# Kernel tuning notes

Hardware: AMD Instinct MI355X
Metric: run time of the kernel (lower is better)

## Reference

```python
import jax, jax.numpy as jnp
import numpy as np

B, IN_CH, D, H, W = 2, 4, 8, 224, 224
DS = 4
DIM, HEADS, HEAD_DIM, LAYERS = 256, 8, 32, 4
INNER = HEADS * HEAD_DIM
MLP = 4 * DIM
WS = (4, 8, 8)
SHIFT = (2, 4, 4)
WVOL = WS[0] * WS[1] * WS[2]
Hp, Wp = H // DS, W // DS
NW = (D // WS[0]) * (Hp // WS[1]) * (Wp // WS[2])
NBIAS = (2 * WS[0] - 1) * (2 * WS[1] - 1) * (2 * WS[2] - 1)


def _rel_index():
    c = np.stack(np.meshgrid(np.arange(WS[0]), np.arange(WS[1]), np.arange(WS[2]), indexing='ij')).reshape(3, -1)
    r = (c[:, :, None] - c[:, None, :]).transpose(1, 2, 0)
    r[..., 0] += WS[0] - 1
    r[..., 1] += WS[1] - 1
    r[..., 2] += WS[2] - 1
    return r[..., 0] * (2 * WS[1] - 1) * (2 * WS[2] - 1) + r[..., 1] * (2 * WS[2] - 1) + r[..., 2]

REL_IDX = jnp.asarray(_rel_index())  # (WVOL, WVOL)


def _shift_mask():
    # standard Swin shifted-window attention mask on the post-merge grid
    img = np.zeros((D, Hp, Wp), np.int32)
    cnt = 0
    sl = lambda w, s: (slice(0, -w), slice(-w, -s), slice(-s, None))
    for sd in sl(WS[0], SHIFT[0]):
        for sh in sl(WS[1], SHIFT[1]):
            for sw in sl(WS[2], SHIFT[2]):
                img[sd, sh, sw] = cnt
                cnt += 1
    m = img.reshape(D // WS[0], WS[0], Hp // WS[1], WS[1], Wp // WS[2], WS[2])
    m = m.transpose(0, 2, 4, 1, 3, 5).reshape(NW, WVOL)
    return jnp.asarray(np.where(m[:, None, :] != m[:, :, None], -1e9, 0.0).astype(np.float32))

ATTN_MASK = _shift_mask()  # (NW, WVOL, WVOL)


def layer_norm(x, s, b):
    mu = x.mean(-1, keepdims=True)
    var = x.var(-1, keepdims=True)
    return (x - mu) / jnp.sqrt(var + 1e-5) * s + b


def window_attention(x, qkv_w, out_w, out_b, bias_tab, shifted):
    # x: (B, D, Hp, Wp, C) channel-last
    if shifted:
        x = jnp.roll(x, (-SHIFT[0], -SHIFT[1], -SHIFT[2]), axis=(1, 2, 3))
    xw = x.reshape(B, D // WS[0], WS[0], Hp // WS[1], WS[1], Wp // WS[2], WS[2], DIM)
    xw = xw.transpose(0, 1, 3, 5, 2, 4, 6, 7).reshape(B, NW, WVOL, DIM)
    qkv = xw @ qkv_w  # (B, NW, WVOL, 3*INNER)
    q, k, v = jnp.split(qkv, 3, axis=-1)
    split = lambda t: t.reshape(B, NW, WVOL, HEADS, HEAD_DIM).transpose(0, 1, 3, 2, 4)
    q = split(q) * (HEAD_DIM ** -0.5)
    k, v = split(k), split(v)
    attn = jnp.einsum('bwhid,bwhjd->bwhij', q, k)  # (B, NW, H, WVOL, WVOL)
    bias = bias_tab[REL_IDX].transpose(2, 0, 1)  # (H, WVOL, WVOL)
    attn = attn + bias
    if shifted:
        attn = attn + ATTN_MASK[None, :, None]
    attn = jax.nn.softmax(attn, axis=-1)
    o = jnp.einsum('bwhij,bwhjd->bwhid', attn, v)
    o = o.transpose(0, 1, 3, 2, 4).reshape(B, NW, WVOL, INNER)
    o = o @ out_w + out_b
    o = o.reshape(B, D // WS[0], Hp // WS[1], Wp // WS[2], WS[0], WS[1], WS[2], DIM)
    o = o.transpose(0, 1, 4, 2, 5, 3, 6, 7).reshape(B, D, Hp, Wp, DIM)
    if shifted:
        o = jnp.roll(o, SHIFT, axis=(1, 2, 3))
    return o


def setup_inputs() -> dict:
    key = jax.random.key(0)
    ks = jax.random.split(key, 12)
    s = 0.02
    return {
        'x': jax.random.normal(ks[0], (B, IN_CH, D, H, W), jnp.float32),
        'conv_w': jax.random.normal(ks[1], (DIM, IN_CH, 1, DS, DS), jnp.float32) * s,
        'conv_b': jnp.zeros((DIM,), jnp.float32),
        'ln1_s': jnp.ones((LAYERS, DIM), jnp.float32),
        'ln1_b': jnp.zeros((LAYERS, DIM), jnp.float32),
        'qkv_w': jax.random.normal(ks[2], (LAYERS, DIM, 3 * INNER), jnp.float32) * s,
        'out_w': jax.random.normal(ks[3], (LAYERS, INNER, DIM), jnp.float32) * s,
        'out_b': jnp.zeros((LAYERS, DIM), jnp.float32),
        'bias_tab': jax.random.normal(ks[4], (LAYERS, NBIAS, HEADS), jnp.float32) * s,
        'ln2_s': jnp.ones((LAYERS, DIM), jnp.float32),
        'ln2_b': jnp.zeros((LAYERS, DIM), jnp.float32),
        'fc1_w': jax.random.normal(ks[5], (LAYERS, DIM, MLP), jnp.float32) * s,
        'fc1_b': jnp.zeros((LAYERS, MLP), jnp.float32),
        'fc2_w': jax.random.normal(ks[6], (LAYERS, MLP, DIM), jnp.float32) * s,
        'fc2_b': jnp.zeros((LAYERS, DIM), jnp.float32),
    }


def reference(x, conv_w, conv_b, ln1_s, ln1_b, qkv_w, out_w, out_b, bias_tab, ln2_s, ln2_b, fc1_w, fc1_b, fc2_w, fc2_b):
    # patch merge: Conv3d kernel (1, DS, DS) stride (1, DS, DS)
    y = jax.lax.conv_general_dilated(
        x, conv_w, window_strides=(1, DS, DS), padding='VALID',
        dimension_numbers=('NCDHW', 'OIDHW', 'NCDHW'))
    y = y + conv_b[None, :, None, None, None]
    y = y.transpose(0, 2, 3, 4, 1)  # (B, D, Hp, Wp, DIM) channel-last
    for i in range(LAYERS):
        shifted = (i % 2 == 1)
        y = y + window_attention(layer_norm(y, ln1_s[i], ln1_b[i]),
                                 qkv_w[i], out_w[i], out_b[i], bias_tab[i], shifted)
        h = layer_norm(y, ln2_s[i], ln2_b[i])
        h = jax.nn.gelu(h @ fc1_w[i] + fc1_b[i]) @ fc2_w[i] + fc2_b[i]
        y = y + h
    return y.transpose(0, 4, 1, 2, 3)  # (B, DIM, D, Hp, Wp)
```

## Files before the change

### kernel.cpp

```cpp
#include <hip/hip_runtime.h>

typedef unsigned short ushort_t;
typedef unsigned int   uint_t;

#define NTOK 50176
#define NWIN 98
#define NBIAS 1575

typedef __attribute__((ext_vector_type(8))) short bf16x8;
typedef __attribute__((ext_vector_type(4))) float floatx4;

static __device__ __forceinline__ float lo2f(uint_t u) { return __uint_as_float(u << 16); }
static __device__ __forceinline__ float hi2f(uint_t u) { return __uint_as_float(u & 0xffff0000u); }
static __device__ __forceinline__ ushort_t f2b(float f) {
    union { float f; uint_t u; } v; v.f = f;
    uint_t u = v.u + 0x7fffu + ((v.u >> 16) & 1u);
    return (ushort_t)(u >> 16);
}

__global__ void transpose_w(const float* __restrict__ src, ushort_t* __restrict__ dst,
                            int K, int N) {
    long base = (long)blockIdx.y * K * N;
    int idx = blockIdx.x * 256 + threadIdx.x;
    if (idx < K * N) {
        int k = idx / N, n = idx - k * N;
        dst[base + (long)n * K + k] = f2b(src[base + idx]);
    }
}

__global__ void cast_bf16(const float* __restrict__ src, ushort_t* __restrict__ dst, int n) {
    int i = blockIdx.x * 256 + threadIdx.x;
    if (i < n) dst[i] = f2b(src[i]);
}

__global__ void gen_btab(const float* __restrict__ bias_tab, float* __restrict__ Btab) {
    int slot = blockIdx.y;
    int layer, cls;
    if (slot == 0)      { layer = 0; cls = 0; }
    else if (slot < 9)  { layer = 1; cls = slot - 1; }
    else if (slot == 9) { layer = 2; cls = 0; }
    else                { layer = 3; cls = slot - 10; }
    int idx = blockIdx.x * 256 + threadIdx.x;
    int hd = idx >> 16;
    int ij = idx & 65535;
    int i = ij >> 8, j = ij & 255;
    int di = i >> 6, hi = (i >> 3) & 7, wi = i & 7;
    int dj = j >> 6, hj = (j >> 3) & 7, wj = j & 7;
    int rel = (di - dj + 3) * 225 + (hi - hj + 7) * 15 + (wi - wj + 7);
    float v = bias_tab[((long)layer * NBIAS + rel) * 8 + hd];
    int cd = cls >> 2, ch = (cls >> 1) & 1, cw = cls & 1;
    int ri = (cd ? (di < 2 ? 1 : 2) : 0) * 9 + (ch ? (hi < 4 ? 1 : 2) : 0) * 3 + (cw ? (wi < 4 ? 1 : 2) : 0);
    int rj = (cd ? (dj < 2 ? 1 : 2) : 0) * 9 + (ch ? (hj < 4 ? 1 : 2) : 0) * 3 + (cw ? (wj < 4 ? 1 : 2) : 0);
    if (ri != rj) v = -1e9f;
    Btab[(long)slot * 524288 + idx] = v * 1.4426950408889634f;
}

__global__ void im2row(const float* __restrict__ X, ushort_t* __restrict__ A) {
    int idx = blockIdx.x * 256 + threadIdx.x;
    int t = idx >> 4;
    int k = idx & 15;
    int ic = k >> 2, kh = k & 3;
    int w = t % 56, h = (t / 56) % 56, d = (t / 3136) % 8, b = t / 25088;
    long xi = (((long)(b * 4 + ic) * 8 + d) * 224 + (h * 4 + kh)) * 224 + w * 4;
    float4 u = *(const float4*)(X + xi);
    ushort_t* ap = A + (long)t * 64 + ic * 16 + kh * 4;
    ap[0] = f2b(u.x); ap[1] = f2b(u.y); ap[2] = f2b(u.z); ap[3] = f2b(u.w);
}

__global__ void ln_kernel(const float* __restrict__ Y, ushort_t* __restrict__ Xn,
                          const float* __restrict__ S, const float* __restrict__ Bb) {
    int wv = threadIdx.x >> 6, lane = threadIdx.x & 63;
    long t = (long)blockIdx.x * 4 + wv;
    const float* y = Y + t * 256;
    float v[4], s = 0.f, s2 = 0.f;
#pragma unroll
    for (int r = 0; r < 4; ++r) { v[r] = y[lane + 64 * r]; s += v[r]; s2 += v[r] * v[r]; }
#pragma unroll
    for (int off = 32; off; off >>= 1) { s += __shfl_xor(s, off, 64); s2 += __shfl_xor(s2, off, 64); }
    float mu = s * (1.f / 256.f);
    float var = s2 * (1.f / 256.f) - mu * mu;
    float rstd = rsqrtf(var + 1e-5f);
#pragma unroll
    for (int r = 0; r < 4; ++r) {
        int c = lane + 64 * r;
        Xn[t * 256 + c] = f2b((v[r] - mu) * rstd * S[c] + Bb[c]);
    }
}

__global__ __launch_bounds__(256, 2) void gemm_bt(
    const ushort_t* __restrict__ A, const ushort_t* __restrict__ BT,
    int M, int N, int K,
    const float* __restrict__ bias, int mode,
    ushort_t* __restrict__ C, float* __restrict__ Y) {
    __shared__ ushort_t As[128 * 32];
    __shared__ ushort_t Bs[128 * 32];
    const int tid = threadIdx.x;
    const int wv = tid >> 6;
    const int lane = tid & 63;
    const int quad = lane >> 4;
    const int l15 = lane & 15;
    const long m0 = (long)blockIdx.x * 128;
    const long n0 = (long)blockIdx.y * 128;
    const int wm = (wv & 1) * 64;
    const int wn = (wv >> 1) * 64;
    const int r_loc = lane >> 2;
    const int k_loc = (lane & 3) * 8;

    floatx4 acc[4][4] = {};

    const ushort_t* Ab = A + m0 * K;
    const ushort_t* Bb = BT + n0 * K;

    for (int kt = 0; kt < K; kt += 32) {
#pragma unroll
        for (int q = 0; q < 2; ++q) {
            int slot = wv * 2 + q;
            int row = slot * 16 + r_loc;
            __builtin_amdgcn_global_load_lds(
                (const __attribute__((address_space(1))) void*)(Ab + (long)row * K + kt + k_loc),
                (__attribute__((address_space(3))) void*)(As + slot * 512), 16, 0, 0);
            __builtin_amdgcn_global_load_lds(
                (const __attribute__((address_space(1))) void*)(Bb + (long)row * K + kt + k_loc),
                (__attribute__((address_space(3))) void*)(Bs + slot * 512), 16, 0, 0);
        }
        __syncthreads();
        bf16x8 af[4], bfr[4];
#pragma unroll
        for (int i = 0; i < 4; ++i) {
            af[i]  = *(const bf16x8*)(As + (wm + i * 16 + l15) * 32 + quad * 8);
            bfr[i] = *(const bf16x8*)(Bs + (wn + i * 16 + l15) * 32 + quad * 8);
        }
#pragma unroll
        for (int mi = 0; mi < 4; ++mi)
#pragma unroll
            for (int ni = 0; ni < 4; ++ni)
                acc[mi][ni] = __builtin_amdgcn_mfma_f32_16x16x32_bf16(af[mi], bfr[ni], acc[mi][ni], 0, 0, 0);
        __syncthreads();
    }

    if (mode == 2) {
#pragma unroll
        for (int mi = 0; mi < 4; ++mi)
#pragma unroll
            for (int ni = 0; ni < 4; ++ni) {
                long col = n0 + wn + ni * 16 + l15;
                float bv = bias[col];
#pragma unroll
                for (int r = 0; r < 4; ++r) {
                    long row = m0 + wm + mi * 16 + quad * 4 + r;
                    Y[row * N + col] += acc[mi][ni][r] + bv;
                }
            }
    } else if (mode == 3) {
#pragma unroll
        for (int mi = 0; mi < 4; ++mi)
#pragma unroll
            for (int ni = 0; ni < 4; ++ni) {
                long col = n0 + wn + ni * 16 + l15;
                float bv = bias[col];
#pragma unroll
                for (int r = 0; r < 4; ++r) {
                    long row = m0 + wm + mi * 16 + quad * 4 + r;
                    Y[row * N + col] = acc[mi][ni][r] + bv;
                }
            }
    } else {
#pragma unroll
        for (int mi = 0; mi < 4; ++mi)
#pragma unroll
            for (int ni = 0; ni < 4; ++ni) {
                long col = n0 + wn + ni * 16 + l15;
                float bv = bias ? bias[col] : 0.f;
#pragma unroll
                for (int r = 0; r < 4; ++r) {
                    long row = m0 + wm + mi * 16 + quad * 4 + r;
                    float v = acc[mi][ni][r] + bv;
                    if (mode == 1) {
                        float x3 = v * v * v;
                        v = 0.5f * v * (1.f + tanhf(0.7978845608028654f * (v + 0.044715f * x3)));
                    }
                    C[row * N + col] = f2b(v);
                }
            }
    }
}

#define PSTR 134
#define VTSTR 266
__global__ __launch_bounds__(256, 3) void attn_mfma(
    const ushort_t* __restrict__ QKV, ushort_t* __restrict__ O,
    const float* __restrict__ Btab, int shifted) {
    __shared__ ushort_t Ks[256 * 32];
    __shared__ ushort_t Vt[32 * VTSTR];
    __shared__ ushort_t Pl[4 * 16 * PSTR];
    __shared__ int tok_s[256];

    const int tid = threadIdx.x;
    const int wv = tid >> 6;
    const int lane = tid & 63;
    const int quad = lane >> 4;
    const int l15 = lane & 15;
    const int wdx = blockIdx.x, hd = blockIdx.y, b = blockIdx.z;
    const int wd = wdx / 49;
    const int wh = (wdx / 7) % 7;
    const int ww = wdx % 7;

    const int cls = shifted ? ((wd << 2) | ((wh == 6) << 1) | (ww == 6)) : 0;
    const float* bt = Btab + ((long)(cls * 8 + hd)) * 65536;

    {
        const int t = tid;
        const int di = t >> 6, hi = (t >> 3) & 7, wi = t & 7;
        const int d = wd * 4 + di, h = wh * 8 + hi, w = ww * 8 + wi;
        int d0 = d, h0 = h, w0 = w;
        if (shifted) { d0 = (d + 2) & 7; h0 = (h + 4) % 56; w0 = (w + 4) % 56; }
        const long tok = ((long)((b * 8 + d0) * 56 + h0)) * 56 + w0;
        tok_s[t] = (int)tok;
        const uint4* kp = (const uint4*)(QKV + tok * 768 + 256 + hd * 32);
        const uint4* vp = (const uint4*)(QKV + tok * 768 + 512 + hd * 32);
        uint4* kd = (uint4*)(Ks + t * 32);
#pragma unroll
        for (int p = 0; p < 4; ++p) kd[p] = kp[p];
#pragma unroll
        for (int p = 0; p < 4; ++p) {
            uint4 vvu = vp[p];
            uint_t uu[4] = {vvu.x, vvu.y, vvu.z, vvu.w};
#pragma unroll
            for (int e = 0; e < 4; ++e) {
                int dd = p * 8 + e * 2;
                Vt[dd * VTSTR + t]       = (ushort_t)(uu[e] & 0xffffu);
                Vt[(dd + 1) * VTSTR + t] = (ushort_t)(uu[e] >> 16);
            }
        }
    }
    __syncthreads();

    const float scale = 0.17677669529663687f * 1.4426950408889634f;
    ushort_t* Pw = Pl + wv * 16 * PSTR;

    for (int rg = 0; rg < 4; ++rg) {
        const int rti = wv * 4 + rg;
        bf16x8 aq;
        {
            int tq = tok_s[rti * 16 + l15];
            const uint4* qp = (const uint4*)(QKV + (long)tq * 768 + hd * 32 + quad * 8);
            union { uint4 u; bf16x8 v; } cv; cv.u = *qp; aq = cv.v;
        }
        const float* bp = bt + (long)(rti * 16 + quad * 4) * 256 + l15;
        floatx4 Sc[16];
        float m4[4] = {-3e38f, -3e38f, -3e38f, -3e38f};
#pragma unroll
        for (int hf = 0; hf < 2; ++hf) {
            float bb[8][4];
#pragma unroll
            for (int n8 = 0; n8 < 8; ++n8)
#pragma unroll
                for (int r = 0; r < 4; ++r)
                    bb[n8][r] = bp[r * 256 + (hf * 8 + n8) * 16];
#pragma unroll
            for (int n8 = 0; n8 < 8; ++n8) {
                const int nt = hf * 8 + n8;
                bf16x8 bk = *(const bf16x8*)(Ks + (nt * 16 + l15) * 32 + quad * 8);
                floatx4 z = {};
                Sc[nt] = __builtin_amdgcn_mfma_f32_16x16x32_bf16(aq, bk, z, 0, 0, 0);
            }
#pragma unroll
            for (int n8 = 0; n8 < 8; ++n8) {
                const int nt = hf * 8 + n8;
#pragma unroll
                for (int r = 0; r < 4; ++r) {
                    float s = fmaf(Sc[nt][r], scale, bb[n8][r]);
                    Sc[nt][r] = s;
                    m4[r] = fmaxf(m4[r], s);
                }
            }
        }
#pragma unroll
        for (int r = 0; r < 4; ++r) {
            m4[r] = fmaxf(m4[r], __shfl_xor(m4[r], 1));
            m4[r] = fmaxf(m4[r], __shfl_xor(m4[r], 2));
            m4[r] = fmaxf(m4[r], __shfl_xor(m4[r], 4));
            m4[r] = fmaxf(m4[r], __shfl_xor(m4[r], 8));
        }
        float l4[4] = {0.f, 0.f, 0.f, 0.f};
#pragma unroll
        for (int nt = 0; nt < 16; ++nt)
#pragma unroll
            for (int r = 0; r < 4; ++r) {
                float p = __builtin_amdgcn_exp2f(Sc[nt][r] - m4[r]);
                l4[r] += p;
                Sc[nt][r] = p;
            }
#pragma unroll
        for (int r = 0; r < 4; ++r) {
            l4[r] += __shfl_xor(l4[r], 1);
            l4[r] += __shfl_xor(l4[r], 2);
            l4[r] += __shfl_xor(l4[r], 4);
            l4[r] += __shfl_xor(l4[r], 8);
        }
        float inv4[4];
#pragma unroll
        for (int r = 0; r < 4; ++r) inv4[r] = 1.f / l4[r];

        floatx4 oa[2] = {};
#pragma unroll
        for (int hf = 0; hf < 2; ++hf) {
#pragma unroll
            for (int n8 = 0; n8 < 8; ++n8)
#pragma unroll
                for (int r = 0; r < 4; ++r)
                    Pw[(quad * 4 + r) * PSTR + n8 * 16 + l15] = f2b(Sc[hf * 8 + n8][r]);
            __builtin_amdgcn_s_waitcnt(0xC07F);
            __builtin_amdgcn_wave_barrier();
#pragma unroll
            for (int ct = 0; ct < 2; ++ct)
#pragma unroll
                for (int kt = 0; kt < 4; ++kt) {
                    bf16x8 ap = *(const bf16x8*)(Pw + l15 * PSTR + kt * 32 + quad * 8);
                    bf16x8 bv = *(const bf16x8*)(Vt + (ct * 16 + l15) * VTSTR + hf * 128 + kt * 32 + quad * 8);
                    oa[ct] = __builtin_amdgcn_mfma_f32_16x16x32_bf16(ap, bv, oa[ct], 0, 0, 0);
                }
            __builtin_amdgcn_s_waitcnt(0xC07F);
            __builtin_amdgcn_wave_barrier();
        }
#pragma unroll
        for (int ct = 0; ct < 2; ++ct)
#pragma unroll
            for (int r = 0; r < 4; ++r) {
                int i = rti * 16 + quad * 4 + r;
                long tq = tok_s[i];
                O[tq * 256 + hd * 32 + ct * 16 + l15] = f2b(oa[ct][r] * inv4[r]);
            }
    }
}

__global__ void out_permute(const float* __restrict__ Y, float* __restrict__ Out) {
    __shared__ float tile[64][65];
    const int t0 = blockIdx.x * 64;
    const int c0 = blockIdx.y * 64;
    const int tid = threadIdx.x;
    const int a = tid >> 6;
    const int bx = tid & 63;
#pragma unroll
    for (int s8 = 0; s8 < 16; ++s8) {
        int tt = a + s8 * 4;
        tile[tt][bx] = Y[(long)(t0 + tt) * 256 + c0 + bx];
    }
    __syncthreads();
#pragma unroll
    for (int s8 = 0; s8 < 16; ++s8) {
        int cc = a + s8 * 4;
        int tok = t0 + bx;
        int bb = tok / 25088;
        int rem = tok - bb * 25088;
        Out[((long)(bb * 256 + c0 + cc)) * 25088 + rem] = tile[bx][cc];
    }
}

extern "C" void kernel_launch(void* const* d_in, const int* in_sizes, int n_in,
                              void* d_out, int out_size, void* d_ws, size_t ws_size,
                              hipStream_t stream) {
    (void)in_sizes; (void)n_in; (void)out_size; (void)ws_size;
    const float* x        = (const float*)d_in[0];
    const float* conv_w   = (const float*)d_in[1];
    const float* conv_b   = (const float*)d_in[2];
    const float* ln1_s    = (const float*)d_in[3];
    const float* ln1_b    = (const float*)d_in[4];
    const float* qkv_w    = (const float*)d_in[5];
    const float* out_w    = (const float*)d_in[6];
    const float* out_b    = (const float*)d_in[7];
    const float* bias_tab = (const float*)d_in[8];
    const float* ln2_s    = (const float*)d_in[9];
    const float* ln2_b    = (const float*)d_in[10];
    const float* fc1_w    = (const float*)d_in[11];
    const float* fc1_b    = (const float*)d_in[12];
    const float* fc2_w    = (const float*)d_in[13];
    const float* fc2_b    = (const float*)d_in[14];
    float* out = (float*)d_out;

    char* ws = (char*)d_ws;
    float*    y    = (float*)ws;    ws += (size_t)NTOK * 256 * 4;
    ushort_t* big  = (ushort_t*)ws; ws += (size_t)NTOK * 1024 * 2;
    ushort_t* xob  = (ushort_t*)ws; ws += (size_t)NTOK * 256 * 2;
    ushort_t* bt_qkv = (ushort_t*)ws; ws += (size_t)4 * 768 * 256 * 2;
    ushort_t* bt_out = (ushort_t*)ws; ws += (size_t)4 * 256 * 256 * 2;
    ushort_t* bt_fc1 = (ushort_t*)ws; ws += (size_t)4 * 1024 * 256 * 2;
    ushort_t* bt_fc2 = (ushort_t*)ws; ws += (size_t)4 * 256 * 1024 * 2;
    ushort_t* cw_bf  = (ushort_t*)ws; ws += (size_t)256 * 64 * 2;
    float*    btab   = (float*)ws;  ws += (size_t)18 * 524288 * 4;

    transpose_w<<<dim3((256 * 768 + 255) / 256, 4), 256, 0, stream>>>(qkv_w, bt_qkv, 256, 768);
    transpose_w<<<dim3((256 * 256 + 255) / 256, 4), 256, 0, stream>>>(out_w, bt_out, 256, 256);
    transpose_w<<<dim3((256 * 1024 + 255) / 256, 4), 256, 0, stream>>>(fc1_w, bt_fc1, 256, 1024);
    transpose_w<<<dim3((1024 * 256 + 255) / 256, 4), 256, 0, stream>>>(fc2_w, bt_fc2, 1024, 256);
    gen_btab<<<dim3(2048, 18), 256, 0, stream>>>(bias_tab, btab);

    cast_bf16<<<(256 * 64 + 255) / 256, 256, 0, stream>>>(conv_w, cw_bf, 256 * 64);
    im2row<<<NTOK * 16 / 256, 256, 0, stream>>>(x, big);
    gemm_bt<<<dim3(NTOK / 128, 2), 256, 0, stream>>>(
        big, cw_bf, NTOK, 256, 64, conv_b, 3, nullptr, y);

    static const int base_slot[4] = {0, 1, 9, 10};
    for (int i = 0; i < 4; ++i) {
        int sh = i & 1;
        ln_kernel<<<NTOK / 4, 256, 0, stream>>>(y, xob, ln1_s + i * 256, ln1_b + i * 256);
        gemm_bt<<<dim3(NTOK / 128, 6), 256, 0, stream>>>(
            xob, bt_qkv + (size_t)i * 768 * 256, NTOK, 768, 256, nullptr, 0, big, nullptr);
        attn_mfma<<<dim3(NWIN, 8, 2), 256, 0, stream>>>(
            big, xob, btab + (size_t)base_slot[i] * 524288, sh);
        gemm_bt<<<dim3(NTOK / 128, 2), 256, 0, stream>>>(
            xob, bt_out + (size_t)i * 256 * 256, NTOK, 256, 256, out_b + i * 256, 2, nullptr, y);
        ln_kernel<<<NTOK / 4, 256, 0, stream>>>(y, xob, ln2_s + i * 256, ln2_b + i * 256);
        gemm_bt<<<dim3(NTOK / 128, 8), 256, 0, stream>>>(
            xob, bt_fc1 + (size_t)i * 1024 * 256, NTOK, 1024, 256, fc1_b + i * 1024, 1, big, nullptr);
        gemm_bt<<<dim3(NTOK / 128, 2), 256, 0, stream>>>(
            big, bt_fc2 + (size_t)i * 256 * 1024, NTOK, 256, 1024, fc2_b + i * 256, 2, nullptr, y);
    }

    out_permute<<<dim3(NTOK / 64, 4), 256, 0, stream>>>(y, out);
}
```

Baseline: 1.424 ms.

## Transpose QK^T MFMA so softmax rows live per lane with packed bf16 P stores

Swaps the MFMA operand order so each lane holds one query row's scores across its four accumulator elements. The row max and sum then need only two cross-lane shuffles instead of sixteen. Bias is loaded as float4 vectors, and P is written to LDS with packed v_cvt_pk_bf16_f32 as 64-bit stores using a tighter row stride. The normalisation factor is redistributed with extra shuffles, and the change to LDS padding may alter bank-conflict behaviour.

```diff
diff --git a/kernel.cpp b/kernel.cpp
--- a/kernel.cpp
+++ b/kernel.cpp
@@ -10,12 +10,15 @@
 typedef __attribute__((ext_vector_type(8))) short bf16x8;
 typedef __attribute__((ext_vector_type(4))) float floatx4;
 
-static __device__ __forceinline__ float lo2f(uint_t u) { return __uint_as_float(u << 16); }
-static __device__ __forceinline__ float hi2f(uint_t u) { return __uint_as_float(u & 0xffff0000u); }
 static __device__ __forceinline__ ushort_t f2b(float f) {
     union { float f; uint_t u; } v; v.f = f;
     uint_t u = v.u + 0x7fffu + ((v.u >> 16) & 1u);
     return (ushort_t)(u >> 16);
+}
+static __device__ __forceinline__ uint_t pk_bf16(float a, float b) {
+    uint_t r;
+    asm("v_cvt_pk_bf16_f32 %0, %1, %2" : "=v"(r) : "v"(a), "v"(b));
+    return r;
 }
 
 __global__ void transpose_w(const float* __restrict__ src, ushort_t* __restrict__ dst,
@@ -185,7 +188,7 @@
     }
 }
 
-#define PSTR 134
+#define PSTR 132
 #define VTSTR 266
 __global__ __launch_bounds__(256, 3) void attn_mfma(
     const ushort_t* __restrict__ QKV, ushort_t* __restrict__ O,
@@ -240,76 +243,62 @@
 
     for (int rg = 0; rg < 4; ++rg) {
         const int rti = wv * 4 + rg;
-        bf16x8 aq;
+        bf16x8 bq;
         {
             int tq = tok_s[rti * 16 + l15];
             const uint4* qp = (const uint4*)(QKV + (long)tq * 768 + hd * 32 + quad * 8);
-            union { uint4 u; bf16x8 v; } cv; cv.u = *qp; aq = cv.v;
-        }
-        const float* bp = bt + (long)(rti * 16 + quad * 4) * 256 + l15;
+            union { uint4 u; bf16x8 v; } cv; cv.u = *qp; bq = cv.v;
+        }
+        const float* bp = bt + ((rti * 16 + l15) << 8) + quad * 4;
         floatx4 Sc[16];
-        float m4[4] = {-3e38f, -3e38f, -3e38f, -3e38f};
+#pragma unroll
+        for (int nt = 0; nt < 16; ++nt) {
+            bf16x8 ak = *(const bf16x8*)(Ks + (nt * 16 + l15) * 32 + quad * 8);
+            floatx4 z = {};
+            Sc[nt] = __builtin_amdgcn_mfma_f32_16x16x32_bf16(ak, bq, z, 0, 0, 0);
+        }
+        float m = -3e38f;
+#pragma unroll
+        for (int nt = 0; nt < 16; ++nt) {
+            floatx4 bb = *(const floatx4*)(bp + nt * 16);
+#pragma unroll
+            for (int r = 0; r < 4; ++r) {
+                float s = fmaf(Sc[nt][r], scale, bb[r]);
+                Sc[nt][r] = s;
+                m = fmaxf(m, s);
+            }
+        }
+        m = fmaxf(m, __shfl_xor(m, 16));
+        m = fmaxf(m, __shfl_xor(m, 32));
+        float l = 0.f;
+#pragma unroll
+        for (int nt = 0; nt < 16; ++nt)
+#pragma unroll
+            for (int r = 0; r < 4; ++r) {
+                float p = __builtin_amdgcn_exp2f(Sc[nt][r] - m);
+                l += p;
+                Sc[nt][r] = p;
+            }
+        l += __shfl_xor(l, 16);
+        l += __shfl_xor(l, 32);
+        float inv = 1.f / l;
+        float invr[4];
+#pragma unroll
+        for (int r = 0; r < 4; ++r)
+            invr[r] = __shfl(inv, quad * 20 + r, 64);
+
+        floatx4 oa[2] = {};
 #pragma unroll
         for (int hf = 0; hf < 2; ++hf) {
-            float bb[8][4];
-#pragma unroll
-            for (int n8 = 0; n8 < 8; ++n8)
-#pragma unroll
-                for (int r = 0; r < 4; ++r)
-                    bb[n8][r] = bp[r * 256 + (hf * 8 + n8) * 16];
-#pragma unroll
-            for (int n8 = 0; n8 < 8; ++n8) {
-                const int nt = hf * 8 + n8;
-                bf16x8 bk = *(const bf16x8*)(Ks + (nt * 16 + l15) * 32 + quad * 8);
-                floatx4 z = {};
-                Sc[nt] = __builtin_amdgcn_mfma_f32_16x16x32_bf16(aq, bk, z, 0, 0, 0);
-            }
-#pragma unroll
-            for (int n8 = 0; n8 < 8; ++n8) {
-                const int nt = hf * 8 + n8;
-#pragma unroll
-                for (int r = 0; r < 4; ++r) {
-                    float s = fmaf(Sc[nt][r], scale, bb[n8][r]);
-                    Sc[nt][r] = s;
-                    m4[r] = fmaxf(m4[r], s);
-                }
-            }
-        }
-#pragma unroll
-        for (int r = 0; r < 4; ++r) {
-            m4[r] = fmaxf(m4[r], __shfl_xor(m4[r], 1));
-            m4[r] = fmaxf(m4[r], __shfl_xor(m4[r], 2));
-            m4[r] = fmaxf(m4[r], __shfl_xor(m4[r], 4));
-            m4[r] = fmaxf(m4[r], __shfl_xor(m4[r], 8));
-        }
-        float l4[4] = {0.f, 0.f, 0.f, 0.f};
-#pragma unroll
-        for (int nt = 0; nt < 16; ++nt)
-#pragma unroll
-            for (int r = 0; r < 4; ++r) {
-                float p = __builtin_amdgcn_exp2f(Sc[nt][r] - m4[r]);
-                l4[r] += p;
-                Sc[nt][r] = p;
-            }
-#pragma unroll
-        for (int r = 0; r < 4; ++r) {
-            l4[r] += __shfl_xor(l4[r], 1);
-            l4[r] += __shfl_xor(l4[r], 2);
-            l4[r] += __shfl_xor(l4[r], 4);
-            l4[r] += __shfl_xor(l4[r], 8);
-        }
-        float inv4[4];
-#pragma unroll
-        for (int r = 0; r < 4; ++r) inv4[r] = 1.f / l4[r];
-
-        floatx4 oa[2] = {};
-#pragma unroll
-        for (int hf = 0; hf < 2; ++hf) {
-#pragma unroll
-            for (int n8 = 0; n8 < 8; ++n8)
-#pragma unroll
-                for (int r = 0; r < 4; ++r)
-                    Pw[(quad * 4 + r) * PSTR + n8 * 16 + l15] = f2b(Sc[hf * 8 + n8][r]);
+            uint_t* pw32 = (uint_t*)(Pw + l15 * PSTR);
+#pragma unroll
+            for (int nt = 0; nt < 8; ++nt) {
+                const int s4 = hf * 8 + nt;
+                uint2 w2;
+                w2.x = pk_bf16(Sc[s4][0], Sc[s4][1]);
+                w2.y = pk_bf16(Sc[s4][2], Sc[s4][3]);
+                *(uint2*)(pw32 + nt * 8 + quad * 2) = w2;
+            }
             __builtin_amdgcn_s_waitcnt(0xC07F);
             __builtin_amdgcn_wave_barrier();
 #pragma unroll
@@ -329,7 +318,7 @@
             for (int r = 0; r < 4; ++r) {
                 int i = rti * 16 + quad * 4 + r;
                 long tq = tok_s[i];
-                O[tq * 256 + hd * 32 + ct * 16 + l15] = f2b(oa[ct][r] * inv4[r]);
+                O[tq * 256 + hd * 32 + ct * 16 + l15] = f2b(oa[ct][r] * invr[r]);
             }
     }
 }
```

Measured after the change: 1.487 ms. +4.4%, slower.

## Fuse LayerNorm into N=256 GEMM epilogues with full-row tiles

Applied to the files above, without the earlier changes.

Adds a gemm_ln kernel in which each block computes a full 128x256 output row tile, so the residual update and the following LayerNorm can be done in the epilogue with shuffle reductions. It replaces the separate ln_kernel launches after the conv, out-projection and fc2 GEMMs, which removes one fp32 read pass over the activations per fusion. In exchange the grid has half as many blocks, each wave holds 32 accumulator vectors, and the epilogue does strided scalar stores, which may lower occupancy and store efficiency.

```diff
diff --git a/kernel.cpp b/kernel.cpp
--- a/kernel.cpp
+++ b/kernel.cpp
@@ -10,8 +10,6 @@
 typedef __attribute__((ext_vector_type(8))) short bf16x8;
 typedef __attribute__((ext_vector_type(4))) float floatx4;
 
-static __device__ __forceinline__ float lo2f(uint_t u) { return __uint_as_float(u << 16); }
-static __device__ __forceinline__ float hi2f(uint_t u) { return __uint_as_float(u & 0xffff0000u); }
 static __device__ __forceinline__ ushort_t f2b(float f) {
     union { float f; uint_t u; } v; v.f = f;
     uint_t u = v.u + 0x7fffu + ((v.u >> 16) & 1u);
@@ -67,26 +65,6 @@
     ap[0] = f2b(u.x); ap[1] = f2b(u.y); ap[2] = f2b(u.z); ap[3] = f2b(u.w);
 }
 
-__global__ void ln_kernel(const float* __restrict__ Y, ushort_t* __restrict__ Xn,
-                          const float* __restrict__ S, const float* __restrict__ Bb) {
-    int wv = threadIdx.x >> 6, lane = threadIdx.x & 63;
-    long t = (long)blockIdx.x * 4 + wv;
-    const float* y = Y + t * 256;
-    float v[4], s = 0.f, s2 = 0.f;
-#pragma unroll
-    for (int r = 0; r < 4; ++r) { v[r] = y[lane + 64 * r]; s += v[r]; s2 += v[r] * v[r]; }
-#pragma unroll
-    for (int off = 32; off; off >>= 1) { s += __shfl_xor(s, off, 64); s2 += __shfl_xor(s2, off, 64); }
-    float mu = s * (1.f / 256.f);
-    float var = s2 * (1.f / 256.f) - mu * mu;
-    float rstd = rsqrtf(var + 1e-5f);
-#pragma unroll
-    for (int r = 0; r < 4; ++r) {
-        int c = lane + 64 * r;
-        Xn[t * 256 + c] = f2b((v[r] - mu) * rstd * S[c] + Bb[c]);
-    }
-}
-
 __global__ __launch_bounds__(256, 2) void gemm_bt(
     const ushort_t* __restrict__ A, const ushort_t* __restrict__ BT,
     int M, int N, int K,
@@ -151,19 +129,6 @@
                     Y[row * N + col] += acc[mi][ni][r] + bv;
                 }
             }
-    } else if (mode == 3) {
-#pragma unroll
-        for (int mi = 0; mi < 4; ++mi)
-#pragma unroll
-            for (int ni = 0; ni < 4; ++ni) {
-                long col = n0 + wn + ni * 16 + l15;
-                float bv = bias[col];
-#pragma unroll
-                for (int r = 0; r < 4; ++r) {
-                    long row = m0 + wm + mi * 16 + quad * 4 + r;
-                    Y[row * N + col] = acc[mi][ni][r] + bv;
-                }
-            }
     } else {
 #pragma unroll
         for (int mi = 0; mi < 4; ++mi)
@@ -182,6 +147,104 @@
                     C[row * N + col] = f2b(v);
                 }
             }
+    }
+}
+
+__global__ __launch_bounds__(256, 2) void gemm_ln(
+    const ushort_t* __restrict__ A, const ushort_t* __restrict__ BT,
+    int M, int K,
+    const float* __restrict__ bias, int mode,
+    const float* __restrict__ ln_s, const float* __restrict__ ln_b,
+    float* __restrict__ Y, ushort_t* __restrict__ Xn) {
+    __shared__ ushort_t As[128 * 32];
+    __shared__ ushort_t Bs[256 * 32];
+    const int tid = threadIdx.x;
+    const int wv = tid >> 6;
+    const int lane = tid & 63;
+    const int quad = lane >> 4;
+    const int l15 = lane & 15;
+    const long m0 = (long)blockIdx.x * 128;
+    const int wm = wv * 32;
+    const int r_loc = lane >> 2;
+    const int k_loc = (lane & 3) * 8;
+
+    floatx4 acc[2][16] = {};
+    const ushort_t* Ab = A + m0 * K;
+
+    for (int kt = 0; kt < K; kt += 32) {
+#pragma unroll
+        for (int q = 0; q < 2; ++q) {
+            int slot = wv * 2 + q;
+            int row = slot * 16 + r_loc;
+            __builtin_amdgcn_global_load_lds(
+                (const __attribute__((address_space(1))) void*)(Ab + (long)row * K + kt + k_loc),
+                (__attribute__((address_space(3))) void*)(As + slot * 512), 16, 0, 0);
+        }
+#pragma unroll
+        for (int q = 0; q < 4; ++q) {
+            int slot = wv * 4 + q;
+            int row = slot * 16 + r_loc;
+            __builtin_amdgcn_global_load_lds(
+                (const __attribute__((address_space(1))) void*)(BT + (long)row * K + kt + k_loc),
+                (__attribute__((address_space(3))) void*)(Bs + slot * 512), 16, 0, 0);
+        }
+        __syncthreads();
+        bf16x8 af0 = *(const bf16x8*)(As + (wm + l15) * 32 + quad * 8);
+        bf16x8 af1 = *(const bf16x8*)(As + (wm + 16 + l15) * 32 + quad * 8);
+#pragma unroll
+        for (int ni = 0; ni < 16; ++ni) {
+            bf16x8 bfr = *(const bf16x8*)(Bs + (ni * 16 + l15) * 32 + quad * 8);
+            acc[0][ni] = __builtin_amdgcn_mfma_f32_16x16x32_bf16(af0, bfr, acc[0][ni], 0, 0, 0);
+            acc[1][ni] = __builtin_amdgcn_mfma_f32_16x16x32_bf16(af1, bfr, acc[1][ni], 0, 0, 0);
+        }
+        __syncthreads();
+    }
+
+    float bv[16], sv[16], bbv[16];
+#pragma unroll
+    for (int ni = 0; ni < 16; ++ni) {
+        int col = ni * 16 + l15;
+        bv[ni] = bias[col];
+        sv[ni] = ln_s[col];
+        bbv[ni] = ln_b[col];
+    }
+
+#pragma unroll
+    for (int mi = 0; mi < 2; ++mi) {
+#pragma unroll
+        for (int ni = 0; ni < 16; ++ni) {
+            int col = ni * 16 + l15;
+#pragma unroll
+            for (int r = 0; r < 4; ++r) {
+                long row = m0 + wm + mi * 16 + quad * 4 + r;
+                float v = acc[mi][ni][r] + bv[ni];
+                if (mode == 2) v += Y[row * 256 + col];
+                Y[row * 256 + col] = v;
+                acc[mi][ni][r] = v;
+            }
+        }
+#pragma unroll
+        for (int r = 0; r < 4; ++r) {
+            float s = 0.f, s2 = 0.f;
+#pragma unroll
+            for (int ni = 0; ni < 16; ++ni) {
+                float v = acc[mi][ni][r];
+                s += v; s2 += v * v;
+            }
+            s += __shfl_xor(s, 1); s2 += __shfl_xor(s2, 1);
+            s += __shfl_xor(s, 2); s2 += __shfl_xor(s2, 2);
+            s += __shfl_xor(s, 4); s2 += __shfl_xor(s2, 4);
+            s += __shfl_xor(s, 8); s2 += __shfl_xor(s2, 8);
+            float mu = s * (1.f / 256.f);
+            float var = s2 * (1.f / 256.f) - mu * mu;
+            float rstd = rsqrtf(var + 1e-5f);
+            long row = m0 + wm + mi * 16 + quad * 4 + r;
+#pragma unroll
+            for (int ni = 0; ni < 16; ++ni) {
+                int col = ni * 16 + l15;
+                Xn[row * 256 + col] = f2b((acc[mi][ni][r] - mu) * rstd * sv[ni] + bbv[ni]);
+            }
+        }
     }
 }
 
@@ -397,24 +460,29 @@
 
     cast_bf16<<<(256 * 64 + 255) / 256, 256, 0, stream>>>(conv_w, cw_bf, 256 * 64);
     im2row<<<NTOK * 16 / 256, 256, 0, stream>>>(x, big);
-    gemm_bt<<<dim3(NTOK / 128, 2), 256, 0, stream>>>(
-        big, cw_bf, NTOK, 256, 64, conv_b, 3, nullptr, y);
+    gemm_ln<<<NTOK / 128, 256, 0, stream>>>(
+        big, cw_bf, NTOK, 64, conv_b, 3, ln1_s, ln1_b, y, xob);
 
     static const int base_slot[4] = {0, 1, 9, 10};
     for (int i = 0; i < 4; ++i) {
         int sh = i & 1;
-        ln_kernel<<<NTOK / 4, 256, 0, stream>>>(y, xob, ln1_s + i * 256, ln1_b + i * 256);
         gemm_bt<<<dim3(NTOK / 128, 6), 256, 0, stream>>>(
             xob, bt_qkv + (size_t)i * 768 * 256, NTOK, 768, 256, nullptr, 0, big, nullptr);
         attn_mfma<<<dim3(NWIN, 8, 2), 256, 0, stream>>>(
             big, xob, btab + (size_t)base_slot[i] * 524288, sh);
-        gemm_bt<<<dim3(NTOK / 128, 2), 256, 0, stream>>>(
-            xob, bt_out + (size_t)i * 256 * 256, NTOK, 256, 256, out_b + i * 256, 2, nullptr, y);
-        ln_kernel<<<NTOK / 4, 256, 0, stream>>>(y, xob, ln2_s + i * 256, ln2_b + i * 256);
+        gemm_ln<<<NTOK / 128, 256, 0, stream>>>(
+            xob, bt_out + (size_t)i * 256 * 256, NTOK, 256, out_b + i * 256, 2,
+            ln2_s + i * 256, ln2_b + i * 256, y, xob);
         gemm_bt<<<dim3(NTOK / 128, 8), 256, 0, stream>>>(
             xob, bt_fc1 + (size_t)i * 1024 * 256, NTOK, 1024, 256, fc1_b + i * 1024, 1, big, nullptr);
-        gemm_bt<<<dim3(NTOK / 128, 2), 256, 0, stream>>>(
-            big, bt_fc2 + (size_t)i * 256 * 1024, NTOK, 256, 1024, fc2_b + i * 256, 2, nullptr, y);
+        if (i < 3) {
+            gemm_ln<<<NTOK / 128, 256, 0, stream>>>(
+                big, bt_fc2 + (size_t)i * 256 * 1024, NTOK, 1024, fc2_b + i * 256, 2,
+                ln1_s + (i + 1) * 256, ln1_b + (i + 1) * 256, y, xob);
+        } else {
+            gemm_bt<<<dim3(NTOK / 128, 2), 256, 0, stream>>>(
+                big, bt_fc2 + (size_t)i * 256 * 1024, NTOK, 256, 1024, fc2_b + i * 256, 2, nullptr, y);
+        }
     }
 
     out_permute<<<dim3(NTOK / 64, 4), 256, 0, stream>>>(y, out);
```

New measurement: 1.488 ms. 1.04x slower.
